# Kernel optimization log

Measured on AMD Instinct MI355X. Metric: run time of the kernel, lower is better.

Reference implementation:

```python
import jax, jax.numpy as jnp
import numpy as np

EPS = 1e-08

def setup_inputs() -> dict:
    key = jax.random.key(0)
    k1, k2 = jax.random.split(key)
    h = jax.random.normal(k1, (4, 4096, 2048), dtype=jnp.float32)
    vectors = jax.random.normal(k2, (16, 2048), dtype=jnp.float32) * 0.01
    return {"h": h, "vectors": vectors}

def reference(h, vectors):
    # Chain of k Householder reflections applied sequentially (loop-carried h).
    def step(h, v):
        v_norm_sq = jnp.maximum(jnp.dot(v, v), EPS)
        proj = jnp.einsum('bsd,d->bs', h, v)  # [B,S]
        h = h - (2.0 / v_norm_sq) * proj[..., None] * v
        return h, None
    h, _ = jax.lax.scan(step, h, vectors)
    return h
```

## Files before the change

### kernel.cpp

```cpp
#include <hip/hip_runtime.h>

#define HH_EPS 1e-8f

constexpr int D     = 2048;
constexpr int K     = 16;
constexpr int RR    = 2;
constexpr int CH    = D / (64 * 4);
constexpr int NROWS = 4 * 4096;
constexpr int TPB   = 1024;
constexpr int WPB   = TPB / 64;
constexpr int SPAD  = 9;

__global__ void __launch_bounds__(64) hh_gram_kernel(const float* __restrict__ vecs,
                                                     float* __restrict__ G) {
    int i = blockIdx.x >> 4, j = blockIdx.x & 15;
    int lane = threadIdx.x;
    const float4* a = (const float4*)(vecs + i * D);
    const float4* b = (const float4*)(vecs + j * D);
    float s = 0.f;
#pragma unroll
    for (int c = 0; c < CH; ++c) {
        float4 x = a[c * 64 + lane], y = b[c * 64 + lane];
        s += x.x * y.x + x.y * y.y + x.z * y.z + x.w * y.w;
    }
#pragma unroll
    for (int off = 32; off >= 1; off >>= 1) s += __shfl_xor(s, off);
    if (lane == 0) G[i * K + j] = s;
}

__global__ void __launch_bounds__(256) hh_buildT_kernel(const float* __restrict__ G,
                                                        float* __restrict__ T) {
    __shared__ float sG[K * K], sT[K * K];
    int t = threadIdx.x;
    sG[t] = G[t]; sT[t] = 0.f;
    __syncthreads();
    for (int k = 0; k < K; ++k) {
        float beta = 2.f / fmaxf(sG[k * K + k], HH_EPS);
        if (t == k) sT[k * K + k] = beta;
        else if (t < k) {
            float s = 0.f;
            for (int j = t; j < k; ++j) s += sT[t * K + j] * sG[j * K + k];
            sT[t * K + k] = -beta * s;
        }
        __syncthreads();
    }
    T[t] = sT[t];
}

__global__ void __launch_bounds__(1024, 4)
hh_apply_wy(const float* __restrict__ h_in, const float* __restrict__ vecs,
            const float* __restrict__ Tmat, float* __restrict__ h_out) {
    __shared__ float4 sv[K * (D / 4)];
    __shared__ float  sP[WPB * RR * K * SPAD];
    __shared__ float  sD[WPB * RR * K];
    __shared__ float  sW[WPB * RR * K];
    __shared__ float  sT[K * K];

    const int t    = threadIdx.x;
    const int wv   = t >> 6;
    const int lane = t & 63;
    const int gw   = blockIdx.x * WPB + wv;
    const size_t rbase = (size_t)gw * RR;

    float4 h[RR][CH];
    const float4* hin4 = (const float4*)h_in;
#pragma unroll
    for (int r = 0; r < RR; ++r)
#pragma unroll
        for (int j = 0; j < CH; ++j)
            h[r][j] = hin4[(rbase + r) * (D / 4) + j * 64 + lane];

    const float4* v4 = (const float4*)vecs;
#pragma unroll
    for (int i = 0; i < K * (D / 4) / TPB; ++i) {
        int idx = t + i * TPB;
        __builtin_amdgcn_global_load_lds(
            (const __attribute__((address_space(1))) unsigned int*)(v4 + idx),
            (__attribute__((address_space(3))) unsigned int*)(sv + idx),
            16, 0, 0);
    }
    if (t < K * K) sT[t] = Tmat[t];
    __syncthreads();

    float* myP = sP + wv * (RR * K * SPAD);
    float* myD = sD + wv * (RR * K);
    float* myW = sW + wv * (RR * K);

#pragma unroll 1
    for (int k = 0; k < K; ++k) {
        float a0x = 0.f, a0y = 0.f, a0z = 0.f, a0w = 0.f;
        float a1x = 0.f, a1y = 0.f, a1z = 0.f, a1w = 0.f;
#pragma unroll
        for (int j = 0; j < CH; ++j) {
            float4 v = sv[k * (D / 4) + j * 64 + lane];
            a0x += h[0][j].x * v.x; a0y += h[0][j].y * v.y;
            a0z += h[0][j].z * v.z; a0w += h[0][j].w * v.w;
            a1x += h[1][j].x * v.x; a1y += h[1][j].y * v.y;
            a1z += h[1][j].z * v.z; a1w += h[1][j].w * v.w;
        }
        float s0 = (a0x + a0y) + (a0z + a0w);
        float s1 = (a1x + a1y) + (a1z + a1w);
        s0 += __shfl_xor(s0, 32); s0 += __shfl_xor(s0, 16); s0 += __shfl_xor(s0, 8);
        s1 += __shfl_xor(s1, 32); s1 += __shfl_xor(s1, 16); s1 += __shfl_xor(s1, 8);
        if (lane < 8) {
            myP[(0 * K + k) * SPAD + lane] = s0;
            myP[(1 * K + k) * SPAD + lane] = s1;
        }
    }

    const int kk  = lane & 15;
    const int seg = lane >> 4;
#pragma unroll
    for (int r = 0; r < RR; ++r) {
        float s = myP[(r * K + kk) * SPAD + seg * 2]
                + myP[(r * K + kk) * SPAD + seg * 2 + 1];
        s += __shfl_xor(s, 16);
        s += __shfl_xor(s, 32);
        if (lane < 16) myD[r * K + kk] = s;
    }

#pragma unroll
    for (int r = 0; r < RR; ++r) {
        float wsum = 0.f;
#pragma unroll
        for (int k2 = 0; k2 < K; ++k2)
            wsum += myD[r * K + k2] * sT[k2 * K + kk];
        if (lane < 16) myW[r * K + kk] = wsum;
    }

#pragma unroll 1
    for (int k = 0; k < K; ++k) {
        const float w0 = myW[0 * K + k];
        const float w1 = myW[1 * K + k];
#pragma unroll
        for (int j = 0; j < CH; ++j) {
            float4 v = sv[k * (D / 4) + j * 64 + lane];
            h[0][j].x -= w0 * v.x; h[0][j].y -= w0 * v.y;
            h[0][j].z -= w0 * v.z; h[0][j].w -= w0 * v.w;
            h[1][j].x -= w1 * v.x; h[1][j].y -= w1 * v.y;
            h[1][j].z -= w1 * v.z; h[1][j].w -= w1 * v.w;
        }
    }

#pragma unroll
    for (int r = 0; r < RR; ++r) {
        float4* row = (float4*)h_out + (rbase + r) * (D / 4);
#pragma unroll
        for (int j = 0; j < CH; ++j)
            row[j * 64 + lane] = h[r][j];
    }
}

extern "C" void kernel_launch(void* const* d_in, const int* in_sizes, int n_in,
                              void* d_out, int out_size, void* d_ws, size_t ws_size,
                              hipStream_t stream) {
    const float* h    = (const float*)d_in[0];
    const float* vecs = (const float*)d_in[1];
    float* out        = (float*)d_out;

    float* G  = (float*)d_ws;
    float* Tm = G + K * K;

    hh_gram_kernel<<<K * K, 64, 0, stream>>>(vecs, G);
    hh_buildT_kernel<<<1, 256, 0, stream>>>(G, Tm);

    int blocks = NROWS / (RR * WPB);
    hh_apply_wy<<<blocks, TPB, 0, stream>>>(h, vecs, Tm, out);
}
```

Baseline: 261.8 us.

## Make WY apply kernel persistent with more rows per wave

The apply kernel becomes persistent: 256 blocks of 512 threads loop over row batches, so the 128KB vector table is staged into LDS once per block instead of once per small block. Each wave now handles 4 rows instead of 2, so every LDS vector load is reused across more rows. The cost is higher register pressure (64 float4 of h state per lane) and lower occupancy, and global loads are no longer overlapped across blocks within a CU.

```diff
diff --git a/kernel.cpp b/kernel.cpp
--- a/kernel.cpp
+++ b/kernel.cpp
@@ -4,11 +4,13 @@
 
 constexpr int D     = 2048;
 constexpr int K     = 16;
-constexpr int RR    = 2;
+constexpr int RR    = 4;
 constexpr int CH    = D / (64 * 4);
 constexpr int NROWS = 4 * 4096;
-constexpr int TPB   = 1024;
+constexpr int TPB   = 512;
 constexpr int WPB   = TPB / 64;
+constexpr int NBLK  = 256;
+constexpr int NBATCH= NROWS / (NBLK * WPB * RR);
 constexpr int SPAD  = 9;
 
 __global__ void __launch_bounds__(64) hh_gram_kernel(const float* __restrict__ vecs,
@@ -47,7 +49,7 @@
     T[t] = sT[t];
 }
 
-__global__ void __launch_bounds__(1024, 4)
+__global__ void __launch_bounds__(512, 2)
 hh_apply_wy(const float* __restrict__ h_in, const float* __restrict__ vecs,
             const float* __restrict__ Tmat, float* __restrict__ h_out) {
     __shared__ float4 sv[K * (D / 4)];
@@ -59,16 +61,6 @@
     const int t    = threadIdx.x;
     const int wv   = t >> 6;
     const int lane = t & 63;
-    const int gw   = blockIdx.x * WPB + wv;
-    const size_t rbase = (size_t)gw * RR;
-
-    float4 h[RR][CH];
-    const float4* hin4 = (const float4*)h_in;
-#pragma unroll
-    for (int r = 0; r < RR; ++r)
-#pragma unroll
-        for (int j = 0; j < CH; ++j)
-            h[r][j] = hin4[(rbase + r) * (D / 4) + j * 64 + lane];
 
     const float4* v4 = (const float4*)vecs;
 #pragma unroll
@@ -86,68 +78,85 @@
     float* myD = sD + wv * (RR * K);
     float* myW = sW + wv * (RR * K);
 
-#pragma unroll 1
-    for (int k = 0; k < K; ++k) {
-        float a0x = 0.f, a0y = 0.f, a0z = 0.f, a0w = 0.f;
-        float a1x = 0.f, a1y = 0.f, a1z = 0.f, a1w = 0.f;
-#pragma unroll
-        for (int j = 0; j < CH; ++j) {
-            float4 v = sv[k * (D / 4) + j * 64 + lane];
-            a0x += h[0][j].x * v.x; a0y += h[0][j].y * v.y;
-            a0z += h[0][j].z * v.z; a0w += h[0][j].w * v.w;
-            a1x += h[1][j].x * v.x; a1y += h[1][j].y * v.y;
-            a1z += h[1][j].z * v.z; a1w += h[1][j].w * v.w;
-        }
-        float s0 = (a0x + a0y) + (a0z + a0w);
-        float s1 = (a1x + a1y) + (a1z + a1w);
-        s0 += __shfl_xor(s0, 32); s0 += __shfl_xor(s0, 16); s0 += __shfl_xor(s0, 8);
-        s1 += __shfl_xor(s1, 32); s1 += __shfl_xor(s1, 16); s1 += __shfl_xor(s1, 8);
-        if (lane < 8) {
-            myP[(0 * K + k) * SPAD + lane] = s0;
-            myP[(1 * K + k) * SPAD + lane] = s1;
-        }
-    }
-
     const int kk  = lane & 15;
     const int seg = lane >> 4;
+
+#pragma unroll 1
+    for (int b = 0; b < NBATCH; ++b) {
+        const int gw = b * (NBLK * WPB) + blockIdx.x * WPB + wv;
+        const size_t rbase = (size_t)gw * RR;
+
+        float4 h[RR][CH];
+        const float4* hin4 = (const float4*)h_in;
 #pragma unroll
-    for (int r = 0; r < RR; ++r) {
-        float s = myP[(r * K + kk) * SPAD + seg * 2]
-                + myP[(r * K + kk) * SPAD + seg * 2 + 1];
-        s += __shfl_xor(s, 16);
-        s += __shfl_xor(s, 32);
-        if (lane < 16) myD[r * K + kk] = s;
-    }
+        for (int r = 0; r < RR; ++r)
+#pragma unroll
+            for (int j = 0; j < CH; ++j)
+                h[r][j] = hin4[(rbase + r) * (D / 4) + j * 64 + lane];
+
+#pragma unroll 1
+        for (int k = 0; k < K; ++k) {
+            float ax[RR], ay[RR], az[RR], aw[RR];
+#pragma unroll
+            for (int r = 0; r < RR; ++r) { ax[r]=0.f; ay[r]=0.f; az[r]=0.f; aw[r]=0.f; }
+#pragma unroll
+            for (int j = 0; j < CH; ++j) {
+                float4 v = sv[k * (D / 4) + j * 64 + lane];
+#pragma unroll
+                for (int r = 0; r < RR; ++r) {
+                    ax[r] += h[r][j].x * v.x; ay[r] += h[r][j].y * v.y;
+                    az[r] += h[r][j].z * v.z; aw[r] += h[r][j].w * v.w;
+                }
+            }
+#pragma unroll
+            for (int r = 0; r < RR; ++r) {
+                float s = (ax[r] + ay[r]) + (az[r] + aw[r]);
+                s += __shfl_xor(s, 32); s += __shfl_xor(s, 16); s += __shfl_xor(s, 8);
+                if (lane < 8) myP[(r * K + k) * SPAD + lane] = s;
+            }
+        }
 
 #pragma unroll
-    for (int r = 0; r < RR; ++r) {
-        float wsum = 0.f;
+        for (int r = 0; r < RR; ++r) {
+            float s = myP[(r * K + kk) * SPAD + seg * 2]
+                    + myP[(r * K + kk) * SPAD + seg * 2 + 1];
+            s += __shfl_xor(s, 16);
+            s += __shfl_xor(s, 32);
+            if (lane < 16) myD[r * K + kk] = s;
+        }
+
 #pragma unroll
-        for (int k2 = 0; k2 < K; ++k2)
-            wsum += myD[r * K + k2] * sT[k2 * K + kk];
-        if (lane < 16) myW[r * K + kk] = wsum;
-    }
+        for (int r = 0; r < RR; ++r) {
+            float wsum = 0.f;
+#pragma unroll
+            for (int k2 = 0; k2 < K; ++k2)
+                wsum += myD[r * K + k2] * sT[k2 * K + kk];
+            if (lane < 16) myW[r * K + kk] = wsum;
+        }
 
 #pragma unroll 1
-    for (int k = 0; k < K; ++k) {
-        const float w0 = myW[0 * K + k];
-        const float w1 = myW[1 * K + k];
+        for (int k = 0; k < K; ++k) {
+            float w[RR];
 #pragma unroll
-        for (int j = 0; j < CH; ++j) {
-            float4 v = sv[k * (D / 4) + j * 64 + lane];
-            h[0][j].x -= w0 * v.x; h[0][j].y -= w0 * v.y;
-            h[0][j].z -= w0 * v.z; h[0][j].w -= w0 * v.w;
-            h[1][j].x -= w1 * v.x; h[1][j].y -= w1 * v.y;
-            h[1][j].z -= w1 * v.z; h[1][j].w -= w1 * v.w;
+            for (int r = 0; r < RR; ++r) w[r] = myW[r * K + k];
+#pragma unroll
+            for (int j = 0; j < CH; ++j) {
+                float4 v = sv[k * (D / 4) + j * 64 + lane];
+#pragma unroll
+                for (int r = 0; r < RR; ++r) {
+                    h[r][j].x -= w[r] * v.x; h[r][j].y -= w[r] * v.y;
+                    h[r][j].z -= w[r] * v.z; h[r][j].w -= w[r] * v.w;
+                }
+            }
         }
-    }
 
 #pragma unroll
-    for (int r = 0; r < RR; ++r) {
-        float4* row = (float4*)h_out + (rbase + r) * (D / 4);
+        for (int r = 0; r < RR; ++r) {
+            float4* row = (float4*)h_out + (rbase + r) * (D / 4);
 #pragma unroll
-        for (int j = 0; j < CH; ++j)
-            row[j * 64 + lane] = h[r][j];
+            for (int j = 0; j < CH; ++j)
+                row[j * 64 + lane] = h[r][j];
+        }
     }
 }
 
@@ -164,6 +173,5 @@
     hh_gram_kernel<<<K * K, 64, 0, stream>>>(vecs, G);
     hh_buildT_kernel<<<1, 256, 0, stream>>>(G, Tm);
 
-    int blocks = NROWS / (RR * WPB);
-    hh_apply_wy<<<blocks, TPB, 0, stream>>>(h, vecs, Tm, out);
+    hh_apply_wy<<<NBLK, TPB, 0, stream>>>(h, vecs, Tm, out);
 }
```

After: 263.4 us. About the same (+0.6%).
